# Optimization experiments

Measured on AMD Instinct MI355X. Metric: run time of the kernel, lower is better.

## Reference

```python
import jax, jax.numpy as jnp
import numpy as np

DIM = 1024
NUM_HEADS = 16
BATCH = 4
SEQ = 2048
SCALE = (DIM // NUM_HEADS) ** -0.5
MASK_VAL = -10000000.0


def setup_inputs() -> dict:
    key = jax.random.key(0)
    k1, k2, k3, k4 = jax.random.split(key, 4)
    inputs = jax.random.normal(k1, (BATCH, SEQ, DIM), dtype=jnp.float32)
    # xavier-ish scaling for weights
    W_qkv = jax.random.normal(k2, (3 * DIM, DIM), dtype=jnp.float32) * (1.0 / np.sqrt(DIM))
    W_fc = jax.random.normal(k3, (DIM, DIM), dtype=jnp.float32) * (1.0 / np.sqrt(DIM))
    b_fc = jnp.zeros((DIM,), dtype=jnp.float32)
    padding_mask = jax.random.randint(k4, (BATCH, SEQ), 0, 2, dtype=jnp.int32)
    return {"inputs": inputs, "W_qkv": W_qkv, "W_fc": W_fc, "b_fc": b_fc,
            "padding_mask": padding_mask}


def reference(inputs, W_qkv, W_fc, b_fc, padding_mask):
    B, N, C = inputs.shape
    H = NUM_HEADS
    Dh = C // H
    # qkv projection (torch Linear: x @ W.T), [B,N,3C]
    qkv = jnp.einsum('bnc,oc->bno', inputs, W_qkv)
    qkv = qkv.reshape(B, N, 3, H, Dh).transpose(2, 0, 3, 1, 4)  # [3,B,H,N,Dh]
    q, k, v = qkv[0], qkv[1], qkv[2]
    att = jnp.einsum('bhqd,bhkd->bhqk', q, k) * SCALE  # [B,H,N,N]
    mask = padding_mask[:, None, None, :]              # [B,1,1,N]
    att = jnp.where(mask > 0, jnp.float32(MASK_VAL), att)
    att = jax.nn.softmax(att, axis=-1)
    x = jnp.einsum('bhqk,bhkd->bhqd', att, v)          # [B,H,N,Dh]
    x = x.transpose(0, 2, 1, 3).reshape(B, N, C)       # [B,N,C]
    out = jnp.einsum('bnc,oc->bno', x, W_fc) + b_fc
    return out
```

## Files before the change

### kernel.cpp

```cpp
#include <hip/hip_runtime.h>
#include <stdint.h>

constexpr int kDim  = 1024;
constexpr int kH    = 16;
constexpr int kB    = 4;
constexpr int kSeq  = 2048;
constexpr int kDh   = 64;
constexpr int kMTot = kB * kSeq;
constexpr int kNQkv = 3 * kDim;
constexpr float kScale = 0.125f;
constexpr float kLog2e = 1.44269504088896f;
constexpr float kC1    = kScale * kLog2e;
constexpr float kMaxSub = 10.0f;
constexpr float kMk2Un   = -kMaxSub * kLog2e;
constexpr float kMk2Mask = -1.0e9f;
constexpr int kPld = 72;

typedef __attribute__((ext_vector_type(8))) short short8;
typedef __attribute__((ext_vector_type(4))) float floatx4;

__device__ __forceinline__ unsigned short f2bf(float f) {
  union { float f; unsigned u; } v; v.f = f;
  unsigned r = v.u + 0x7fffu + ((v.u >> 16) & 1u);
  return (unsigned short)(r >> 16);
}
__device__ __forceinline__ unsigned short f2bf_fast(float f) {
  union { float f; unsigned u; } v; v.f = f;
  return (unsigned short)((v.u + 0x8000u) >> 16);
}
__device__ __forceinline__ float vexp2(float x) {
  float r; asm("v_exp_f32 %0, %1" : "=v"(r) : "v"(x)); return r;
}
__device__ __forceinline__ void gl2lds16(const void* g, void* l) {
  __builtin_amdgcn_global_load_lds(
      (const __attribute__((address_space(1))) unsigned int*)g,
      (__attribute__((address_space(3))) unsigned int*)l, 16, 0, 0);
}

__global__ void __launch_bounds__(256) scan_mask(
    const int* __restrict__ pm, int* __restrict__ cidx, int* __restrict__ nkd) {
  const int b = blockIdx.x;
  const int t = threadIdx.x;
  const int lane = t & 63, wv = t >> 6;
  __shared__ int wsum[4];
  __shared__ int woff[5];
  int base = t * 8;
  int keep[8]; int cnt = 0;
#pragma unroll
  for (int j = 0; j < 8; j++) {
    keep[j] = (pm[b * kSeq + base + j] <= 0) ? 1 : 0;
    cnt += keep[j];
  }
  int pre = cnt;
#pragma unroll
  for (int off = 1; off < 64; off <<= 1) {
    int v = __shfl_up(pre, off, 64);
    if (lane >= off) pre += v;
  }
  int excl = pre - cnt;
  if (lane == 63) wsum[wv] = pre;
  __syncthreads();
  if (t == 0) {
    int s = 0;
#pragma unroll
    for (int w = 0; w < 4; w++) { woff[w] = s; s += wsum[w]; }
    woff[4] = s;
    nkd[b] = s;
  }
  __syncthreads();
  const int nk = woff[4];
  int kp = woff[wv] + excl;
#pragma unroll
  for (int j = 0; j < 8; j++) {
    int n = base + j;
    int pos = keep[j] ? kp : nk + (n - kp);
    cidx[b * kSeq + pos] = b * kSeq + n;
    kp += keep[j];
  }
}

__global__ void __launch_bounds__(256) cvt_all(
    const float4* __restrict__ x, const float4* __restrict__ wq,
    const float4* __restrict__ wf,
    ushort4* __restrict__ xb, ushort4* __restrict__ wqb, ushort4* __restrict__ wfb) {
  const int X4  = (kMTot * kDim) / 4;
  const int WQ4 = (kNQkv * kDim) / 4;
  int i = blockIdx.x * 256 + threadIdx.x;
  float4 v; ushort4* dst;
  if (i < X4)            { v = x[i];             dst = xb  + i; }
  else if (i < X4 + WQ4) { v = wq[i - X4];       dst = wqb + (i - X4); }
  else                   { v = wf[i - X4 - WQ4]; dst = wfb + (i - X4 - WQ4); }
  ushort4 o;
  o.x = f2bf(v.x); o.y = f2bf(v.y); o.z = f2bf(v.z); o.w = f2bf(v.w);
  *dst = o;
}

__device__ __forceinline__ void gemm128_mainloop(
    const unsigned short* const arow[4], const unsigned short* __restrict__ Bw,
    int tN, unsigned short* As, unsigned short* Bs, floatx4 acc[4][4]) {
  const int t = threadIdx.x;
  const int lane = t & 63, wv = t >> 6;
  const int wm = (wv >> 1) << 6, wn = (wv & 1) << 6;
  const int lrow = lane & 15, quad = lane >> 4, l7 = lane & 7;
  const int srow = t >> 3;
  const int pu8 = (t & 7) * 8;
  const int lu8 = ((t & 7) ^ (srow & 7)) * 8;
  const int off0 = (quad ^ l7) * 8;

  floatx4 zero = {0.f, 0.f, 0.f, 0.f};
#pragma unroll
  for (int mi = 0; mi < 4; mi++)
#pragma unroll
    for (int ni = 0; ni < 4; ni++) acc[mi][ni] = zero;

  for (int k0 = 0; k0 < kDim; k0 += 64) {
#pragma unroll
    for (int p = 0; p < 4; ++p) {
      int r = srow + p * 32;
      gl2lds16(arow[p] + k0 + lu8, As + r * 64 + pu8);
      gl2lds16(Bw + (int64_t)(tN + r) * kDim + k0 + lu8, Bs + r * 64 + pu8);
    }
    __syncthreads();
#pragma unroll
    for (int kk = 0; kk < 64; kk += 32) {
      short8 af[4], bf[4];
#pragma unroll
      for (int mi = 0; mi < 4; mi++)
        af[mi] = *(const short8*)(As + (wm + mi * 16 + lrow) * 64 + (off0 ^ kk));
#pragma unroll
      for (int ni = 0; ni < 4; ni++)
        bf[ni] = *(const short8*)(Bs + (wn + ni * 16 + lrow) * 64 + (off0 ^ kk));
#pragma unroll
      for (int mi = 0; mi < 4; mi++)
#pragma unroll
        for (int ni = 0; ni < 4; ni++)
          acc[mi][ni] = __builtin_amdgcn_mfma_f32_16x16x32_bf16(af[mi], bf[ni], acc[mi][ni], 0, 0, 0);
    }
    __syncthreads();
  }
}

__global__ void __launch_bounds__(256) gemm_qkv(
    const unsigned short* __restrict__ xb, const unsigned short* __restrict__ wqb,
    const int* __restrict__ cidx, const int* __restrict__ nkd,
    unsigned short* __restrict__ qb, unsigned short* __restrict__ kb,
    unsigned short* __restrict__ vtb) {
  const int tN = blockIdx.x * 128, tM = blockIdx.y * 128;
  const int which = tN >> 10;
  if (which != 0) {
    int b = tM >> 11, local = tM & 2047;
    if (local >= nkd[b]) return;
  }
  __shared__ __attribute__((aligned(16))) unsigned short As[128 * 64];
  __shared__ __attribute__((aligned(16))) unsigned short Bs[128 * 64];
  floatx4 acc[4][4];

  const int t = threadIdx.x, srow = t >> 3;
  const unsigned short* arow[4];
#pragma unroll
  for (int p = 0; p < 4; p++) {
    int r = tM + srow + p * 32;
    int rid = (which == 0) ? r : cidx[r];
    arow[p] = xb + (int64_t)rid * kDim;
  }
  gemm128_mainloop(arow, wqb, tN, As, Bs, acc);

  const int lane = t & 63, wv = t >> 6;
  const int wm = (wv >> 1) << 6, wn = (wv & 1) << 6;
  const int lrow = lane & 15, quad = lane >> 4;
#pragma unroll
  for (int ni = 0; ni < 4; ni++) {
    int o0 = tN + wn + ni * 16;
    int h = (o0 >> 6) & 15;
    int d = (o0 & 63) + lrow;
#pragma unroll
    for (int mi = 0; mi < 4; mi++) {
#pragma unroll
      for (int r = 0; r < 4; r++) {
        int i = tM + wm + mi * 16 + quad * 4 + r;
        int bb = i >> 11, n = i & 2047;
        int64_t base = (int64_t)((bb << 4) + h) << 17;
        unsigned short val = f2bf(acc[mi][ni][r]);
        if (which == 0)      qb [base + (int64_t)n * 64 + d]   = val;
        else if (which == 1) kb [base + (int64_t)n * 64 + d]   = val;
        else                 vtb[base + (int64_t)d * 2048 + n] = val;
      }
    }
  }
}

__global__ void __launch_bounds__(256, 4) attn(
    const unsigned short* __restrict__ qb, const unsigned short* __restrict__ kb,
    const unsigned short* __restrict__ vtb, const int* __restrict__ nkd,
    unsigned short* __restrict__ xab) {
  __shared__ __attribute__((aligned(16))) unsigned short Ks[64 * 64];
  __shared__ __attribute__((aligned(16))) unsigned short Vs[64 * 64];
  __shared__ __attribute__((aligned(16))) unsigned short Ps[4][2][16 * kPld];
  __shared__ float smask[64];

  const int t = threadIdx.x, lane = t & 63, wv = t >> 6;
  const int lrow = lane & 15, quad = lane >> 4, l7 = lane & 7;
  const int qblk = blockIdx.x & 15, bh = blockIdx.x >> 4;
  const int b = bh >> 4, h = bh & 15;
  const int q0 = qblk * 128;
  const int srow = t >> 3;
  const int pu8 = (t & 7) * 8;
  const int lu8 = ((t & 7) ^ (srow & 7)) * 8;
  const int off0 = (quad ^ l7) * 8;

  const int nk  = nkd[b];
  const int nkt = (nk + 63) >> 6;

  const unsigned short* Qb0 = qb + ((int64_t)bh * kSeq + q0 + wv * 16 + lrow) * kDh;
  short8 qf[2][2];
  qf[0][0] = *(const short8*)(Qb0 + quad * 8);
  qf[0][1] = *(const short8*)(Qb0 + 32 + quad * 8);
  qf[1][0] = *(const short8*)(Qb0 + 64 * kDh + quad * 8);
  qf[1][1] = *(const short8*)(Qb0 + 64 * kDh + 32 + quad * 8);

  float l_run[2][4];
  floatx4 o_acc[2][4];
  floatx4 zero = {0.f, 0.f, 0.f, 0.f};
#pragma unroll
  for (int t2 = 0; t2 < 2; t2++) {
#pragma unroll
    for (int r = 0; r < 4; r++) l_run[t2][r] = 0.f;
#pragma unroll
    for (int di = 0; di < 4; di++) o_acc[t2][di] = zero;
  }

  const unsigned short* Kbase = kb  + (int64_t)bh * kSeq * kDh;
  const unsigned short* Vbase = vtb + (int64_t)bh * kDh * kSeq;

  for (int kt = 0; kt < nkt; ++kt) {
    const int k0 = kt * 64;
    {
      int r0 = srow, r1 = srow + 32;
      gl2lds16(Kbase + (int64_t)(k0 + r0) * kDh + lu8, Ks + r0 * 64 + pu8);
      gl2lds16(Kbase + (int64_t)(k0 + r1) * kDh + lu8, Ks + r1 * 64 + pu8);
      gl2lds16(Vbase + (int64_t)r0 * kSeq + k0 + lu8,  Vs + r0 * 64 + pu8);
      gl2lds16(Vbase + (int64_t)r1 * kSeq + k0 + lu8,  Vs + r1 * 64 + pu8);
    }
    if (t < 64) smask[t] = (k0 + t < nk) ? kMk2Un : kMk2Mask;
    __syncthreads();

    floatx4 s[2][4];
#pragma unroll
    for (int ni = 0; ni < 4; ni++) {
      const unsigned short* Kr = Ks + (ni * 16 + lrow) * 64;
      short8 kf0 = *(const short8*)(Kr + off0);
      short8 kf1 = *(const short8*)(Kr + (off0 ^ 32));
#pragma unroll
      for (int t2 = 0; t2 < 2; t2++) {
        floatx4 tmp = __builtin_amdgcn_mfma_f32_16x16x32_bf16(qf[t2][0], kf0, zero, 0, 0, 0);
        s[t2][ni]   = __builtin_amdgcn_mfma_f32_16x16x32_bf16(qf[t2][1], kf1, tmp, 0, 0, 0);
      }
    }
    float mk2[4];
#pragma unroll
    for (int c = 0; c < 4; c++) mk2[c] = smask[c * 16 + lrow];

#pragma unroll
    for (int t2 = 0; t2 < 2; t2++) {
      unsigned short* Pw = &Ps[wv][t2][0];
#pragma unroll
      for (int r = 0; r < 4; r++) {
        int prow = (quad * 4 + r) * kPld + lrow;
#pragma unroll
        for (int c = 0; c < 4; c++) {
          float p = vexp2(fmaf(s[t2][c][r], kC1, mk2[c]));
          l_run[t2][r] += p;
          Pw[prow + c * 16] = f2bf_fast(p);
        }
      }
    }
    asm volatile("s_waitcnt lgkmcnt(0)" ::: "memory");

#pragma unroll
    for (int ks = 0; ks < 2; ks++) {
      short8 pf0 = *(const short8*)(&Ps[wv][0][0] + lrow * kPld + ks * 32 + quad * 8);
      short8 pf1 = *(const short8*)(&Ps[wv][1][0] + lrow * kPld + ks * 32 + quad * 8);
      const int voff = off0 ^ (ks * 32);
#pragma unroll
      for (int di = 0; di < 4; di++) {
        short8 vf = *(const short8*)(Vs + (di * 16 + lrow) * 64 + voff);
        o_acc[0][di] = __builtin_amdgcn_mfma_f32_16x16x32_bf16(pf0, vf, o_acc[0][di], 0, 0, 0);
        o_acc[1][di] = __builtin_amdgcn_mfma_f32_16x16x32_bf16(pf1, vf, o_acc[1][di], 0, 0, 0);
      }
    }
    __syncthreads();
  }

#pragma unroll
  for (int t2 = 0; t2 < 2; t2++) {
#pragma unroll
    for (int r = 0; r < 4; r++) {
      float l = l_run[t2][r];
      l += __shfl_xor(l, 1, 64);
      l += __shfl_xor(l, 2, 64);
      l += __shfl_xor(l, 4, 64);
      l += __shfl_xor(l, 8, 64);
      float inv = 1.0f / l;
      int n = q0 + t2 * 64 + wv * 16 + quad * 4 + r;
      int64_t rowbase = ((int64_t)b * kSeq + n) * kDim + h * kDh;
#pragma unroll
      for (int di = 0; di < 4; di++)
        xab[rowbase + di * 16 + lrow] = f2bf(o_acc[t2][di][r] * inv);
    }
  }
}

__global__ void __launch_bounds__(256) gemm_fc(
    const unsigned short* __restrict__ xab, const unsigned short* __restrict__ wfb,
    const float* __restrict__ bfc, float* __restrict__ out) {
  __shared__ __attribute__((aligned(16))) unsigned short As[128 * 64];
  __shared__ __attribute__((aligned(16))) unsigned short Bs[128 * 64];
  floatx4 acc[4][4];
  const int tN = blockIdx.x * 128, tM = blockIdx.y * 128;
  const int t = threadIdx.x, srow = t >> 3;
  const unsigned short* arow[4];
#pragma unroll
  for (int p = 0; p < 4; p++)
    arow[p] = xab + (int64_t)(tM + srow + p * 32) * kDim;
  gemm128_mainloop(arow, wfb, tN, As, Bs, acc);

  const int lane = t & 63, wv = t >> 6;
  const int wm = (wv >> 1) << 6, wn = (wv & 1) << 6;
  const int lrow = lane & 15, quad = lane >> 4;
#pragma unroll
  for (int ni = 0; ni < 4; ni++) {
    int o = tN + wn + ni * 16 + lrow;
    float bias = bfc[o];
#pragma unroll
    for (int mi = 0; mi < 4; mi++) {
#pragma unroll
      for (int r = 0; r < 4; r++) {
        int i = tM + wm + mi * 16 + quad * 4 + r;
        out[(int64_t)i * kDim + o] = acc[mi][ni][r] + bias;
      }
    }
  }
}

extern "C" void kernel_launch(void* const* d_in, const int* in_sizes, int n_in,
                              void* d_out, int out_size, void* d_ws, size_t ws_size,
                              hipStream_t stream) {
  (void)in_sizes; (void)n_in; (void)out_size; (void)ws_size;
  const float* x    = (const float*)d_in[0];
  const float* wqkv = (const float*)d_in[1];
  const float* wfc  = (const float*)d_in[2];
  const float* bfc  = (const float*)d_in[3];
  const int*   pm   = (const int*)d_in[4];
  float* out = (float*)d_out;

  char* ws = (char*)d_ws;
  unsigned short* xb  = (unsigned short*)(ws);
  unsigned short* wqb = (unsigned short*)(ws + 16777216);
  unsigned short* wfb = (unsigned short*)(ws + 23068672);
  unsigned short* qb  = (unsigned short*)(ws + 25165824);
  unsigned short* kb  = (unsigned short*)(ws + 41943040);
  unsigned short* vtb = (unsigned short*)(ws + 58720256);
  int*            cidx= (int*)(ws + 75497472);
  int*            nkd = (int*)(ws + 75530240);
  unsigned short* xab = xb;

  scan_mask<<<kB, 256, 0, stream>>>(pm, cidx, nkd);
  cvt_all<<<12288, 256, 0, stream>>>((const float4*)x, (const float4*)wqkv,
                                     (const float4*)wfc,
                                     (ushort4*)xb, (ushort4*)wqb, (ushort4*)wfb);
  gemm_qkv<<<dim3(kNQkv / 128, kMTot / 128), 256, 0, stream>>>(xb, wqb, cidx, nkd,
                                                               qb, kb, vtb);
  attn<<<kB * kH * (kSeq / 128), 256, 0, stream>>>(qb, kb, vtb, nkd, xab);
  gemm_fc<<<dim3(kDim / 128, kMTot / 128), 256, 0, stream>>>(xab, wfb, bfc, out);
}
```

Measured before the change: 245.9 us.

## Stage QKV epilogue through LDS for vectorized stores; merge mask scan into convert

The QKV GEMM epilogue now writes its bf16 results into a padded shared-memory tile and then issues 16-byte vector stores to Q/K and to transposed V. Before, each thread stored scattered 2-byte values, and the V-transpose writes were strided. The mask-scan kernel is folded into the conversion kernel as four extra blocks, removing one launch. The attention kernel computes the key mask inline instead of going through shared memory, dropping a store and read. In exchange, the GEMM epilogue adds an extra barrier and LDS traffic, and it uses dynamic shared memory sized 128*136*2 bytes.

```diff
diff --git a/kernel.cpp b/kernel.cpp
--- a/kernel.cpp
+++ b/kernel.cpp
@@ -15,6 +15,7 @@
 constexpr float kMk2Un   = -kMaxSub * kLog2e;
 constexpr float kMk2Mask = -1.0e9f;
 constexpr int kPld = 72;
+constexpr int kCld = 136;
 
 typedef __attribute__((ext_vector_type(8))) short short8;
 typedef __attribute__((ext_vector_type(4))) float floatx4;
@@ -37,54 +38,55 @@
       (__attribute__((address_space(3))) unsigned int*)l, 16, 0, 0);
 }
 
-__global__ void __launch_bounds__(256) scan_mask(
-    const int* __restrict__ pm, int* __restrict__ cidx, int* __restrict__ nkd) {
-  const int b = blockIdx.x;
-  const int t = threadIdx.x;
-  const int lane = t & 63, wv = t >> 6;
-  __shared__ int wsum[4];
-  __shared__ int woff[5];
-  int base = t * 8;
-  int keep[8]; int cnt = 0;
-#pragma unroll
-  for (int j = 0; j < 8; j++) {
-    keep[j] = (pm[b * kSeq + base + j] <= 0) ? 1 : 0;
-    cnt += keep[j];
-  }
-  int pre = cnt;
-#pragma unroll
-  for (int off = 1; off < 64; off <<= 1) {
-    int v = __shfl_up(pre, off, 64);
-    if (lane >= off) pre += v;
-  }
-  int excl = pre - cnt;
-  if (lane == 63) wsum[wv] = pre;
-  __syncthreads();
-  if (t == 0) {
-    int s = 0;
-#pragma unroll
-    for (int w = 0; w < 4; w++) { woff[w] = s; s += wsum[w]; }
-    woff[4] = s;
-    nkd[b] = s;
-  }
-  __syncthreads();
-  const int nk = woff[4];
-  int kp = woff[wv] + excl;
-#pragma unroll
-  for (int j = 0; j < 8; j++) {
-    int n = base + j;
-    int pos = keep[j] ? kp : nk + (n - kp);
-    cidx[b * kSeq + pos] = b * kSeq + n;
-    kp += keep[j];
-  }
-}
-
-__global__ void __launch_bounds__(256) cvt_all(
+__global__ void __launch_bounds__(256) cvt_scan(
     const float4* __restrict__ x, const float4* __restrict__ wq,
     const float4* __restrict__ wf,
-    ushort4* __restrict__ xb, ushort4* __restrict__ wqb, ushort4* __restrict__ wfb) {
+    ushort4* __restrict__ xb, ushort4* __restrict__ wqb, ushort4* __restrict__ wfb,
+    const int* __restrict__ pm, int* __restrict__ cidx, int* __restrict__ nkd) {
   const int X4  = (kMTot * kDim) / 4;
   const int WQ4 = (kNQkv * kDim) / 4;
+  const int NCVT = 12288;
+  if (blockIdx.x >= NCVT) {
+    const int b = blockIdx.x - NCVT;
+    const int t = threadIdx.x;
+    const int lane = t & 63, wv = t >> 6;
+    __shared__ int wsum[4];
+    __shared__ int woff[5];
+    int base = t * 8;
+    int keep[8]; int cnt = 0;
+#pragma unroll
+    for (int j = 0; j < 8; j++) {
+      keep[j] = (pm[b * kSeq + base + j] <= 0) ? 1 : 0;
+      cnt += keep[j];
+    }
+    int pre = cnt;
+#pragma unroll
+    for (int off = 1; off < 64; off <<= 1) {
+      int v = __shfl_up(pre, off, 64);
+      if (lane >= off) pre += v;
+    }
+    int excl = pre - cnt;
+    if (lane == 63) wsum[wv] = pre;
+    __syncthreads();
+    if (t == 0) {
+      int s = 0;
+#pragma unroll
+      for (int w = 0; w < 4; w++) { woff[w] = s; s += wsum[w]; }
+      woff[4] = s;
+      nkd[b] = s;
+    }
+    __syncthreads();
+    const int nk = woff[4];
+    int kp = woff[wv] + excl;
+#pragma unroll
+    for (int j = 0; j < 8; j++) {
+      int n = base + j;
+      int pos = keep[j] ? kp : nk + (n - kp);
+      cidx[b * kSeq + pos] = b * kSeq + n;
+      kp += keep[j];
+    }
+    return;
+  }
   int i = blockIdx.x * 256 + threadIdx.x;
   float4 v; ushort4* dst;
   if (i < X4)            { v = x[i];             dst = xb  + i; }
@@ -151,8 +153,9 @@
     int b = tM >> 11, local = tM & 2047;
     if (local >= nkd[b]) return;
   }
-  __shared__ __attribute__((aligned(16))) unsigned short As[128 * 64];
-  __shared__ __attribute__((aligned(16))) unsigned short Bs[128 * 64];
+  extern __shared__ __attribute__((aligned(16))) unsigned short smem[];
+  unsigned short* As = smem;
+  unsigned short* Bs = smem + 128 * 64;
   floatx4 acc[4][4];
 
   const int t = threadIdx.x, srow = t >> 3;
@@ -168,22 +171,47 @@
   const int lane = t & 63, wv = t >> 6;
   const int wm = (wv >> 1) << 6, wn = (wv & 1) << 6;
   const int lrow = lane & 15, quad = lane >> 4;
+  unsigned short* Cs = smem;
+  const bool vblk = (which == 2);
 #pragma unroll
   for (int ni = 0; ni < 4; ni++) {
-    int o0 = tN + wn + ni * 16;
-    int h = (o0 >> 6) & 15;
-    int d = (o0 & 63) + lrow;
+    int c = wn + ni * 16 + lrow;
 #pragma unroll
     for (int mi = 0; mi < 4; mi++) {
 #pragma unroll
       for (int r = 0; r < 4; r++) {
-        int i = tM + wm + mi * 16 + quad * 4 + r;
+        int row = wm + mi * 16 + quad * 4 + r;
+        unsigned short val = f2bf(acc[mi][ni][r]);
+        if (!vblk) Cs[row * kCld + c] = val;
+        else       Cs[c * kCld + row] = val;
+      }
+    }
+  }
+  __syncthreads();
+  const int mj8 = lane >> 3;
+  const int chunk = lane & 7;
+#pragma unroll
+  for (int half = 0; half < 2; half++) {
+#pragma unroll
+    for (int g = 0; g < 4; g++) {
+      int mjr = wv * 32 + g * 8 + mj8;
+      short8 vec = *(const short8*)(Cs + mjr * kCld + half * 64 + chunk * 8);
+      if (!vblk) {
+        int i = tM + mjr;
         int bb = i >> 11, n = i & 2047;
+        int o = tN + half * 64 + chunk * 8;
+        int h = (o >> 6) & 15;
         int64_t base = (int64_t)((bb << 4) + h) << 17;
-        unsigned short val = f2bf(acc[mi][ni][r]);
-        if (which == 0)      qb [base + (int64_t)n * 64 + d]   = val;
-        else if (which == 1) kb [base + (int64_t)n * 64 + d]   = val;
-        else                 vtb[base + (int64_t)d * 2048 + n] = val;
+        unsigned short* dst = (which == 0 ? qb : kb) + base + (int64_t)n * 64 + (o & 63);
+        *(short8*)dst = vec;
+      } else {
+        int o = tN + mjr;
+        int h = (o >> 6) & 15, d = o & 63;
+        int bb = tM >> 11;
+        int n0 = (tM & 2047) + half * 64 + chunk * 8;
+        unsigned short* dst = vtb + (((int64_t)((bb << 4) + h)) << 17)
+                              + (int64_t)d * 2048 + n0;
+        *(short8*)dst = vec;
       }
     }
   }
@@ -196,7 +224,6 @@
   __shared__ __attribute__((aligned(16))) unsigned short Ks[64 * 64];
   __shared__ __attribute__((aligned(16))) unsigned short Vs[64 * 64];
   __shared__ __attribute__((aligned(16))) unsigned short Ps[4][2][16 * kPld];
-  __shared__ float smask[64];
 
   const int t = threadIdx.x, lane = t & 63, wv = t >> 6;
   const int lrow = lane & 15, quad = lane >> 4, l7 = lane & 7;
@@ -241,7 +268,6 @@
       gl2lds16(Vbase + (int64_t)r0 * kSeq + k0 + lu8,  Vs + r0 * 64 + pu8);
       gl2lds16(Vbase + (int64_t)r1 * kSeq + k0 + lu8,  Vs + r1 * 64 + pu8);
     }
-    if (t < 64) smask[t] = (k0 + t < nk) ? kMk2Un : kMk2Mask;
     __syncthreads();
 
     floatx4 s[2][4];
@@ -258,7 +284,8 @@
     }
     float mk2[4];
 #pragma unroll
-    for (int c = 0; c < 4; c++) mk2[c] = smask[c * 16 + lrow];
+    for (int c = 0; c < 4; c++)
+      mk2[c] = (k0 + c * 16 + lrow < nk) ? kMk2Un : kMk2Mask;
 
 #pragma unroll
     for (int t2 = 0; t2 < 2; t2++) {
@@ -364,12 +391,11 @@
   int*            nkd = (int*)(ws + 75530240);
   unsigned short* xab = xb;
 
-  scan_mask<<<kB, 256, 0, stream>>>(pm, cidx, nkd);
-  cvt_all<<<12288, 256, 0, stream>>>((const float4*)x, (const float4*)wqkv,
-                                     (const float4*)wfc,
-                                     (ushort4*)xb, (ushort4*)wqb, (ushort4*)wfb);
-  gemm_qkv<<<dim3(kNQkv / 128, kMTot / 128), 256, 0, stream>>>(xb, wqb, cidx, nkd,
-                                                               qb, kb, vtb);
+  cvt_scan<<<12288 + kB, 256, 0, stream>>>(
+      (const float4*)x, (const float4*)wqkv, (const float4*)wfc,
+      (ushort4*)xb, (ushort4*)wqb, (ushort4*)wfb, pm, cidx, nkd);
+  gemm_qkv<<<dim3(kNQkv / 128, kMTot / 128), 256, 128 * kCld * 2, stream>>>(
+      xb, wqb, cidx, nkd, qb, kb, vtb);
   attn<<<kB * kH * (kSeq / 128), 256, 0, stream>>>(qb, kb, vtb, nkd, xab);
   gemm_fc<<<dim3(kDim / 128, kMTot / 128), 256, 0, stream>>>(xab, wfb, bfc, out);
 }
```

Result: no change. 242.8 us (-1.3%).
